# Optimization experiments

Measured on AMD Instinct MI355X. Metric: run time of the kernel, lower is better.

## Reference

```python
import jax, jax.numpy as jnp
import numpy as np

N, DIM, OUT, E = 10000, 256, 256, 320000


def setup_inputs() -> dict:
    key = jax.random.key(0)
    ks = jax.random.split(key, 10)
    def w(k, shape):
        fan_in = shape[0]
        return jax.random.normal(k, shape, jnp.float32) * (fan_in ** -0.5)
    return {
        "v_c": jax.random.normal(ks[0], (N, DIM), jnp.float32),
        # row-normalized-ish random adjacency weights so A @ v stays O(1)
        "A": jax.random.uniform(ks[1], (N, N), jnp.float32) * (2.0 / N),
        "src": jax.random.randint(ks[2], (E,), 0, N, jnp.int32),
        "dst": jax.random.randint(ks[3], (E,), 0, N, jnp.int32),
        # ResidualBlock params: lin1 (dim -> 2dim), lin2 (2dim -> dim)
        "W1": w(ks[4], (DIM, 2 * DIM)), "b1": jnp.zeros((2 * DIM,), jnp.float32),
        "W2": w(ks[5], (2 * DIM, DIM)), "b2": jnp.zeros((DIM,), jnp.float32),
        # LatticeMP_Block lin1 / lin2 (dim -> out_dim)
        "Wl1": w(ks[6], (DIM, OUT)), "bl1": jnp.zeros((OUT,), jnp.float32),
        "Wl2": w(ks[7], (DIM, OUT)), "bl2": jnp.zeros((OUT,), jnp.float32),
    }


def reference(v_c, A, src, dst, W1, b1, W2, b2, Wl1, bl1, Wl2, bl2):
    # ResidualBlock: relu(h + lin2(relu(lin1(h))))
    h1 = jnp.maximum(v_c @ W1 + b1, 0.0) @ W2 + b2          # [N, DIM]
    v = jnp.maximum(v_c + h1, 0.0)                           # [N, DIM]
    # relu(lin1(v)) + relu(lin2(A @ v))
    v = jnp.maximum(v @ Wl1 + bl1, 0.0) + jnp.maximum((A @ v) @ Wl2 + bl2, 0.0)  # [N, OUT]
    # DGL update_all(copy_u, sum): h_N[d] = sum_{(s,d) in E} v[s]
    h_N = jax.ops.segment_sum(v[src], dst, num_segments=N)   # [N, OUT]
    return h_N + v
```

## Files before the change

### kernel.cpp

```cpp
#include <hip/hip_runtime.h>
#include <stdint.h>

#define NN 10000
#define DIMV 256
#define HID 512
#define NEDGE 320000
#define SPLIT 6
#define KCH 1664
#define NKT 313
#define APL 2112
#define ABUF 8448
#define BOFF 16896
#define LDSZ 49664

typedef __attribute__((ext_vector_type(8))) short bf16x8;
typedef __attribute__((ext_vector_type(4))) float f32x4;
typedef __attribute__((ext_vector_type(4))) unsigned short u16x4;
typedef __attribute__((ext_vector_type(2))) unsigned int u32x2;

__device__ __forceinline__ unsigned short f2bf(float f) {
  union { float f; unsigned int u; } c; c.f = f;
  return (unsigned short)((c.u + 0x7FFFu + ((c.u >> 16) & 1u)) >> 16);
}
__device__ __forceinline__ float bf2f(unsigned short h) {
  union { unsigned int u; float f; } c; c.u = ((unsigned int)h) << 16;
  return c.f;
}

__device__ __forceinline__ bf16x8 bzero8() {
  bf16x8 r;
#pragma unroll
  for (int i = 0; i < 8; ++i) r[i] = 0;
  return r;
}

__device__ __forceinline__ bf16x8 pack8(const float* x) {
  bf16x8 r;
#pragma unroll
  for (int i = 0; i < 8; ++i) r[i] = (short)f2bf(x[i]);
  return r;
}

__device__ __forceinline__ u32x2 cvt4v(const f32x4 a) {
  u32x2 r;
  asm("v_cvt_pk_bf16_f32 %0, %1, %2" : "=v"(r[0]) : "v"(a[0]), "v"(a[1]));
  asm("v_cvt_pk_bf16_f32 %0, %1, %2" : "=v"(r[1]) : "v"(a[2]), "v"(a[3]));
  return r;
}

typedef __attribute__((address_space(1))) unsigned int gu32;
typedef __attribute__((address_space(3))) unsigned int lu32;
__device__ __forceinline__ void glds16(const void* g, void* l) {
  __builtin_amdgcn_global_load_lds((const gu32*)g, (lu32*)l, 16, 0, 0);
}

__global__ void k_conv(const float* __restrict__ W1, const float* __restrict__ W2,
                       const float* __restrict__ Wl1, const float* __restrict__ Wl2,
                       unsigned short* __restrict__ W1T, unsigned short* __restrict__ W2T,
                       unsigned short* __restrict__ Wl1T, unsigned short* __restrict__ Wl2T,
                       unsigned short* __restrict__ vB, int* __restrict__ counts) {
  int i = blockIdx.x * 256 + threadIdx.x;
  if (i < 131072) {
    { int k = i >> 9, o = i & 511; W1T[o * 256 + k] = f2bf(W1[i]); }
    { int k = i >> 8, o = i & 255; W2T[o * 512 + k] = f2bf(W2[i]); }
    if (i < 65536) {
      int k = i >> 8, o = i & 255;
      Wl1T[o * 256 + k] = f2bf(Wl1[i]);
      Wl2T[o * 256 + k] = f2bf(Wl2[i]);
    }
    if (i < 4096) {
      int c = i >> 4, kk = 16 + (i & 15);
      int g = kk >> 3;
      int byte = c * 64 + ((g ^ ((c >> 1) & 3)) << 4) + (kk & 7) * 2;
      *(unsigned short*)((char*)vB + (size_t)312 * 16384 + byte) = 0;
    }
    if (i < NN) counts[i] = 0;
  }
}

__launch_bounds__(256, 2)
__global__ void k_mlp(const float* __restrict__ vc,
                      const unsigned short* __restrict__ W1T, const float* __restrict__ b1,
                      const unsigned short* __restrict__ W2T, const float* __restrict__ b2,
                      unsigned short* __restrict__ v_rm, unsigned short* __restrict__ vB) {
  __shared__ __align__(16) char sm[65536];
  const int t = threadIdx.x;
  const int lane = t & 63, wid = t >> 6;
  const int wr = wid & 1, wc = wid >> 1;
  const int r0 = blockIdx.x * 32;

  {
    const int row = t >> 3, grow = r0 + row;
#pragma unroll
    for (int q = 0; q < 4; ++q) {
      const int slot = (t & 7) * 4 + q;
      float buf[8] = {0.f, 0.f, 0.f, 0.f, 0.f, 0.f, 0.f, 0.f};
      if (grow < NN) {
        const float4 x0 = *(const float4*)(vc + (size_t)grow * DIMV + slot * 8);
        const float4 x1 = *(const float4*)(vc + (size_t)grow * DIMV + slot * 8 + 4);
        buf[0] = x0.x; buf[1] = x0.y; buf[2] = x0.z; buf[3] = x0.w;
        buf[4] = x1.x; buf[5] = x1.y; buf[6] = x1.z; buf[7] = x1.w;
      }
      *(bf16x8*)(sm + row * 512 + ((slot ^ (row & 7)) * 16)) = pack8(buf);
    }
  }

  f32x4 acc1[16];
#pragma unroll
  for (int i = 0; i < 16; ++i) acc1[i] = (f32x4){0.f, 0.f, 0.f, 0.f};

  for (int step = 0; step < 8; ++step) {
    __syncthreads();
#pragma unroll
    for (int rr = 0; rr < 2; ++rr) {
      const int c = t + rr * 256;
      const unsigned short* srcp = W1T + c * 256 + step * 32;
#pragma unroll
      for (int q = 0; q < 4; ++q) {
        bf16x8 w = *(const bf16x8*)(srcp + q * 8);
        *(bf16x8*)(sm + 16384 + c * 64 + ((q ^ ((c >> 1) & 3)) * 16)) = w;
      }
    }
    __syncthreads();
    const int arow = 16 * wr + (lane & 15);
    const int aslot = step * 4 + (lane >> 4);
    const bf16x8 af = *(const bf16x8*)(sm + arow * 512 + ((aslot ^ (arow & 7)) * 16));
#pragma unroll
    for (int ct = 0; ct < 16; ++ct) {
      const int c = 256 * wc + 16 * ct + (lane & 15);
      const bf16x8 bfr =
          *(const bf16x8*)(sm + 16384 + c * 64 + ((((lane >> 4)) ^ ((c >> 1) & 3)) * 16));
      acc1[ct] = __builtin_amdgcn_mfma_f32_16x16x32_bf16(af, bfr, acc1[ct], 0, 0, 0);
    }
  }
  __syncthreads();
#pragma unroll
  for (int ct = 0; ct < 16; ++ct) {
    const int c = 256 * wc + 16 * ct + (lane & 15);
    const float bb = b1[c];
#pragma unroll
    for (int r = 0; r < 4; ++r) {
      const int row = 16 * wr + (lane >> 4) * 4 + r;
      float v = fmaxf(acc1[ct][r] + bb, 0.f);
      const int slot = c >> 3;
      *(unsigned short*)(sm + 16384 + row * 1024 + ((slot ^ (row & 7)) * 16) + (c & 7) * 2) =
          f2bf(v);
    }
  }

  f32x4 acc2[8];
#pragma unroll
  for (int i = 0; i < 8; ++i) acc2[i] = (f32x4){0.f, 0.f, 0.f, 0.f};

  for (int step = 0; step < 16; ++step) {
    __syncthreads();
    {
      const int c = t;
      const unsigned short* srcp = W2T + c * 512 + step * 32;
#pragma unroll
      for (int q = 0; q < 4; ++q) {
        bf16x8 w = *(const bf16x8*)(srcp + q * 8);
        *(bf16x8*)(sm + 49152 + c * 64 + ((q ^ ((c >> 1) & 3)) * 16)) = w;
      }
    }
    __syncthreads();
    const int arow = 16 * wr + (lane & 15);
    const int aslot = step * 4 + (lane >> 4);
    const bf16x8 af = *(const bf16x8*)(sm + 16384 + arow * 1024 + ((aslot ^ (arow & 7)) * 16));
#pragma unroll
    for (int ct = 0; ct < 8; ++ct) {
      const int c = 128 * wc + 16 * ct + (lane & 15);
      const bf16x8 bfr =
          *(const bf16x8*)(sm + 49152 + c * 64 + ((((lane >> 4)) ^ ((c >> 1) & 3)) * 16));
      acc2[ct] = __builtin_amdgcn_mfma_f32_16x16x32_bf16(af, bfr, acc2[ct], 0, 0, 0);
    }
  }

  const int growbase = r0 + 16 * wr + (lane >> 4) * 4;
  if (growbase < NN) {
#pragma unroll
    for (int ct = 0; ct < 8; ++ct) {
      const int c = 128 * wc + 16 * ct + (lane & 15);
      const float bb = b2[c];
      u16x4 pk;
#pragma unroll
      for (int r = 0; r < 4; ++r) {
        const int grow = growbase + r;
        float v = acc2[ct][r] + bb + vc[(size_t)grow * DIMV + c];
        v = fmaxf(v, 0.f);
        const unsigned short hv = f2bf(v);
        v_rm[(size_t)grow * DIMV + c] = hv;
        pk[r] = hv;
      }
      const int tile = growbase >> 5, kk0 = growbase & 31;
      const int g = kk0 >> 3;
      const int byte = c * 64 + ((g ^ ((c >> 1) & 3)) << 4) + (kk0 & 7) * 2;
      *(u16x4*)((char*)vB + (size_t)tile * 16384 + byte) = pk;
    }
  }
}

__launch_bounds__(512, 4)
__global__ void k_av(const float* __restrict__ A, const unsigned short* __restrict__ vB,
                     unsigned short* __restrict__ avpb) {
  __shared__ __align__(16) char sm[LDSZ];
  const int t = threadIdx.x, lane = t & 63, wid = t >> 6;
  const int wr = wid >> 2, wc = wid & 3;

  const int orig = blockIdx.x;
  const int xcd = orig & 7, idx = orig >> 3;
  const int g = (xcd < 2) ? xcd * 60 + idx : 120 + (xcd - 2) * 59 + idx;
  const int s = g / 79;
  const int xb = g - s * 79;
  const int r0 = xb * 128;
  const int kbase = s * KCH;
  const int tile0 = s * 52;
  const int nst = (s == SPLIT - 1) ? 53 : 52;
  unsigned short* outp = avpb + (size_t)s * NN * DIMV;

  const int srow = t >> 3, sQ = t & 7;
  const float* ap0 = A + (size_t)min(r0 + srow, NN - 1) * NN;
  const float* ap1 = A + (size_t)min(r0 + 64 + srow, NN - 1) * NN;
  const int wbase = (sQ >> 1) * APL + (sQ & 1) * 8;
  const int w0 = wbase + srow * 16;
  const int w1 = wbase + (64 + srow) * 16;

  f32x4 aR0, aR1;

#define AISSUE(ST)                                            \
  do {                                                        \
    int kq = kbase + (ST)*32 + sQ * 4;                        \
    kq = min(kq, 9996);         \
    aR0 = *(const f32x4*)(ap0 + kq);                          \
    aR1 = *(const f32x4*)(ap1 + kq);                          \
  } while (0)

#define AWRITE(BUF)                                           \
  do {                                                        \
    char* wb = sm + (BUF)*ABUF;                               \
    *(u32x2*)(wb + w0) = cvt4v(aR0);                          \
    *(u32x2*)(wb + w1) = cvt4v(aR1);                          \
  } while (0)

#define BSTAGE(BUF, TILE)                                                     \
  do {                                                                        \
    char* lb = sm + BOFF + (BUF)*16384 + wid * 1024;                          \
    const char* gp = (const char*)vB + (size_t)(TILE)*16384 + wid * 1024 +    \
                     lane * 16;                                               \
    glds16(gp, lb);                                                           \
    glds16(gp + 8192, lb + 8192);                                             \
  } while (0)

  f32x4 acc[4][4];
#pragma unroll
  for (int i = 0; i < 4; ++i)
#pragma unroll
    for (int j = 0; j < 4; ++j) acc[i][j] = (f32x4){0.f, 0.f, 0.f, 0.f};

  const int rbase = (lane >> 4) * APL + (wr * 64 + (lane & 15)) * 16;
  int boff[4];
#pragma unroll
  for (int ct = 0; ct < 4; ++ct) {
    const int col = wc * 64 + ct * 16 + (lane & 15);
    boff[ct] = col * 64 + (((lane >> 4) ^ ((col >> 1) & 3)) << 4);
  }

#define COMPUTE(CUR)                                                                 \
  do {                                                                              \
    const char* ab = sm + (CUR)*ABUF;                                               \
    const char* bb = sm + BOFF + (CUR)*16384;                                       \
    const bf16x8 af0 = *(const bf16x8*)(ab + rbase);                                \
    const bf16x8 af1 = *(const bf16x8*)(ab + rbase + 256);                          \
    const bf16x8 af2 = *(const bf16x8*)(ab + rbase + 512);                          \
    const bf16x8 af3 = *(const bf16x8*)(ab + rbase + 768);                          \
    _Pragma("unroll") for (int ct = 0; ct < 4; ++ct) {                              \
      const bf16x8 bfr = *(const bf16x8*)(bb + boff[ct]);                           \
      acc[0][ct] = __builtin_amdgcn_mfma_f32_16x16x32_bf16(af0, bfr, acc[0][ct], 0, 0, 0); \
      acc[1][ct] = __builtin_amdgcn_mfma_f32_16x16x32_bf16(af1, bfr, acc[1][ct], 0, 0, 0); \
      acc[2][ct] = __builtin_amdgcn_mfma_f32_16x16x32_bf16(af2, bfr, acc[2][ct], 0, 0, 0); \
      acc[3][ct] = __builtin_amdgcn_mfma_f32_16x16x32_bf16(af3, bfr, acc[3][ct], 0, 0, 0); \
    }                                                                               \
  } while (0)

  AISSUE(0);
  AWRITE(0);
  BSTAGE(0, tile0);
  __syncthreads();

  int cur = 0;
  for (int st = 0; st < nst; ++st) {
    const bool more = (st + 1 < nst);
    if (more) {
      AISSUE(st + 1);
      BSTAGE(cur ^ 1, tile0 + st + 1);
    }
    COMPUTE(cur);
    if (more) AWRITE(cur ^ 1);
    __syncthreads();
    cur ^= 1;
  }
#undef AISSUE
#undef AWRITE
#undef BSTAGE
#undef COMPUTE

#pragma unroll
  for (int rt = 0; rt < 4; ++rt) {
    const int gb = r0 + wr * 64 + rt * 16 + (lane >> 4) * 4;
    if (gb < NN) {
#pragma unroll
      for (int ct = 0; ct < 4; ++ct) {
        const int col = wc * 64 + ct * 16 + (lane & 15);
#pragma unroll
        for (int r = 0; r < 4; ++r)
          outp[(size_t)(gb + r) * DIMV + col] = f2bf(acc[rt][ct][r]);
      }
    }
  }
}

__launch_bounds__(256, 2)
__global__ void k_out(const unsigned short* __restrict__ v_rm,
                      const unsigned short* __restrict__ avpb,
                      const unsigned short* __restrict__ Wl1T, const float* __restrict__ bl1,
                      const unsigned short* __restrict__ Wl2T, const float* __restrict__ bl2,
                      unsigned short* __restrict__ v2b, float* __restrict__ outb) {
  __shared__ __align__(16) char sm[65536];
  const int t = threadIdx.x, lane = t & 63, wid = t >> 6;
  const int wr = wid & 1, wc = wid >> 1;
  const int r0 = blockIdx.x * 32;

  {
    const int row = t >> 3, grow = r0 + row;
#pragma unroll
    for (int q = 0; q < 4; ++q) {
      const int slot = (t & 7) * 4 + q;
      bf16x8 w = (grow < NN) ? *(const bf16x8*)(v_rm + (size_t)grow * DIMV + slot * 8) : bzero8();
      *(bf16x8*)(sm + row * 512 + ((slot ^ (row & 7)) * 16)) = w;
    }
#pragma unroll
    for (int q = 0; q < 4; ++q) {
      const int slot = (t & 7) * 4 + q;
      float buf[8] = {0.f, 0.f, 0.f, 0.f, 0.f, 0.f, 0.f, 0.f};
      if (grow < NN) {
#pragma unroll
        for (int p = 0; p < SPLIT; ++p) {
          const bf16x8 a =
              *(const bf16x8*)(avpb + (size_t)p * NN * DIMV + (size_t)grow * DIMV + slot * 8);
#pragma unroll
          for (int z = 0; z < 8; ++z) buf[z] += bf2f((unsigned short)a[z]);
        }
      }
      *(bf16x8*)(sm + 16384 + row * 512 + ((slot ^ (row & 7)) * 16)) = pack8(buf);
    }
  }

  f32x4 acc1[8], acc2[8];
#pragma unroll
  for (int i = 0; i < 8; ++i) {
    acc1[i] = (f32x4){0.f, 0.f, 0.f, 0.f};
    acc2[i] = (f32x4){0.f, 0.f, 0.f, 0.f};
  }

  for (int step = 0; step < 8; ++step) {
    __syncthreads();
    {
      const int c = t;
      const unsigned short* s1 = Wl1T + c * 256 + step * 32;
      const unsigned short* s2 = Wl2T + c * 256 + step * 32;
#pragma unroll
      for (int q = 0; q < 4; ++q) {
        const int ps = (q ^ ((c >> 1) & 3)) * 16;
        *(bf16x8*)(sm + 32768 + c * 64 + ps) = *(const bf16x8*)(s1 + q * 8);
        *(bf16x8*)(sm + 49152 + c * 64 + ps) = *(const bf16x8*)(s2 + q * 8);
      }
    }
    __syncthreads();
    const int arow = 16 * wr + (lane & 15);
    const int aslot = step * 4 + (lane >> 4);
    const bf16x8 a1 = *(const bf16x8*)(sm + arow * 512 + ((aslot ^ (arow & 7)) * 16));
    const bf16x8 a2 = *(const bf16x8*)(sm + 16384 + arow * 512 + ((aslot ^ (arow & 7)) * 16));
#pragma unroll
    for (int ct = 0; ct < 8; ++ct) {
      const int c = 128 * wc + 16 * ct + (lane & 15);
      const int bs = (((lane >> 4)) ^ ((c >> 1) & 3)) * 16;
      acc1[ct] = __builtin_amdgcn_mfma_f32_16x16x32_bf16(
          a1, *(const bf16x8*)(sm + 32768 + c * 64 + bs), acc1[ct], 0, 0, 0);
      acc2[ct] = __builtin_amdgcn_mfma_f32_16x16x32_bf16(
          a2, *(const bf16x8*)(sm + 49152 + c * 64 + bs), acc2[ct], 0, 0, 0);
    }
  }

  const int growbase = r0 + 16 * wr + (lane >> 4) * 4;
  if (growbase < NN) {
#pragma unroll
    for (int ct = 0; ct < 8; ++ct) {
      const int c = 128 * wc + 16 * ct + (lane & 15);
      const float u1 = bl1[c], u2 = bl2[c];
#pragma unroll
      for (int r = 0; r < 4; ++r) {
        const float x = fmaxf(acc1[ct][r] + u1, 0.f) + fmaxf(acc2[ct][r] + u2, 0.f);
        v2b[(size_t)(growbase + r) * DIMV + c] = f2bf(x);
        outb[(size_t)(growbase + r) * DIMV + c] = x;
      }
    }
  }
}

__global__ void k_hist(const int* __restrict__ dst, int* __restrict__ counts) {
  const int e = blockIdx.x * 256 + threadIdx.x;
  if (e < NEDGE) atomicAdd(&counts[dst[e]], 1);
}

__global__ void k_scan(const int* __restrict__ counts, int* __restrict__ offsets,
                       int* __restrict__ cursor) {
  __shared__ int wred[16];
  __shared__ int chtot;
  const int t = threadIdx.x;
  const int lane = t & 63, wid = t >> 6;
  int carry = 0;
  for (int base = 0; base < NN; base += 1024) {
    const int i = base + t;
    const int x = (i < NN) ? counts[i] : 0;
    int v = x;
#pragma unroll
    for (int d = 1; d < 64; d <<= 1) {
      int y = __shfl_up(v, d);
      if (lane >= d) v += y;
    }
    if (lane == 63) wred[wid] = v;
    __syncthreads();
    if (t < 16) {
      int sv = wred[t];
#pragma unroll
      for (int d = 1; d < 16; d <<= 1) {
        int y = __shfl_up(sv, d);
        if (t >= d) sv += y;
      }
      wred[t] = sv;
      if (t == 15) chtot = sv;
    }
    __syncthreads();
    const int woff = wid ? wred[wid - 1] : 0;
    const int excl = carry + woff + v - x;
    if (i < NN) { offsets[i] = excl; cursor[i] = excl; }
    carry += chtot;
    __syncthreads();
  }
  if (t == 0) offsets[NN] = carry;
}

__global__ void k_fill(const int* __restrict__ src, const int* __restrict__ dst,
                       int* __restrict__ cursor, int* __restrict__ srcbuf) {
  const int e = blockIdx.x * 256 + threadIdx.x;
  if (e < NEDGE) {
    const int pos = atomicAdd(&cursor[dst[e]], 1);
    srcbuf[pos] = src[e];
  }
}

__launch_bounds__(256)
__global__ void k_gather(const unsigned short* __restrict__ v2b,
                         const int* __restrict__ offsets,
                         const int* __restrict__ srcbuf, float* __restrict__ outb) {
  const int n = (blockIdx.x * 256 + threadIdx.x) >> 6;
  if (n >= NN) return;
  const int lane = threadIdx.x & 63;
  const int beg = offsets[n], end = offsets[n + 1];
  float4 a0 = {0.f, 0.f, 0.f, 0.f}, a1 = a0, a2 = a0, a3 = a0;
  int j = beg;
  for (; j + 4 <= end; j += 4) {
    const int s0 = srcbuf[j], s1 = srcbuf[j + 1], s2 = srcbuf[j + 2], s3 = srcbuf[j + 3];
    const u16x4 x0 = *(const u16x4*)(v2b + (size_t)s0 * DIMV + lane * 4);
    const u16x4 x1 = *(const u16x4*)(v2b + (size_t)s1 * DIMV + lane * 4);
    const u16x4 x2 = *(const u16x4*)(v2b + (size_t)s2 * DIMV + lane * 4);
    const u16x4 x3 = *(const u16x4*)(v2b + (size_t)s3 * DIMV + lane * 4);
    a0.x += bf2f(x0[0]); a0.y += bf2f(x0[1]); a0.z += bf2f(x0[2]); a0.w += bf2f(x0[3]);
    a1.x += bf2f(x1[0]); a1.y += bf2f(x1[1]); a1.z += bf2f(x1[2]); a1.w += bf2f(x1[3]);
    a2.x += bf2f(x2[0]); a2.y += bf2f(x2[1]); a2.z += bf2f(x2[2]); a2.w += bf2f(x2[3]);
    a3.x += bf2f(x3[0]); a3.y += bf2f(x3[1]); a3.z += bf2f(x3[2]); a3.w += bf2f(x3[3]);
  }
  for (; j < end; ++j) {
    const int s0 = srcbuf[j];
    const u16x4 x0 = *(const u16x4*)(v2b + (size_t)s0 * DIMV + lane * 4);
    a0.x += bf2f(x0[0]); a0.y += bf2f(x0[1]); a0.z += bf2f(x0[2]); a0.w += bf2f(x0[3]);
  }
  a0.x += a1.x + a2.x + a3.x; a0.y += a1.y + a2.y + a3.y;
  a0.z += a1.z + a2.z + a3.z; a0.w += a1.w + a2.w + a3.w;
  float* o = outb + (size_t)n * DIMV + lane * 4;
  float4 cur = *(const float4*)o;
  cur.x += a0.x; cur.y += a0.y; cur.z += a0.z; cur.w += a0.w;
  *(float4*)o = cur;
}

extern "C" void kernel_launch(void* const* d_in, const int* in_sizes, int n_in,
                              void* d_out, int out_size, void* d_ws, size_t ws_size,
                              hipStream_t stream) {
  const float* vc  = (const float*)d_in[0];
  const float* A   = (const float*)d_in[1];
  const int*   src = (const int*)d_in[2];
  const int*   dst = (const int*)d_in[3];
  const float* W1  = (const float*)d_in[4];
  const float* b1  = (const float*)d_in[5];
  const float* W2  = (const float*)d_in[6];
  const float* b2  = (const float*)d_in[7];
  const float* Wl1 = (const float*)d_in[8];
  const float* bl1 = (const float*)d_in[9];
  const float* Wl2 = (const float*)d_in[10];
  const float* bl2 = (const float*)d_in[11];
  float* outb = (float*)d_out;
  char* ws = (char*)d_ws;

  unsigned short* W1T  = (unsigned short*)(ws + 0);
  unsigned short* W2T  = (unsigned short*)(ws + 262144);
  unsigned short* Wl1T = (unsigned short*)(ws + 524288);
  unsigned short* Wl2T = (unsigned short*)(ws + 655360);
  unsigned short* vB   = (unsigned short*)(ws + 786432);
  unsigned short* v_rm = (unsigned short*)(ws + 5914624);
  int* counts  = (int*)(ws + 11034624);
  int* offsets = (int*)(ws + 11075584);
  int* cursor  = (int*)(ws + 11116544);
  int* srcbuf  = (int*)(ws + 11157504);
  unsigned short* avpb = (unsigned short*)(ws + 12437760);
  unsigned short* v2b  = (unsigned short*)(ws + 43157760);

  hipLaunchKernelGGL(k_conv, dim3(512), dim3(256), 0, stream,
                     W1, W2, Wl1, Wl2, W1T, W2T, Wl1T, Wl2T, vB, counts);
  hipLaunchKernelGGL(k_hist, dim3((NEDGE + 255) / 256), dim3(256), 0, stream, dst, counts);
  hipLaunchKernelGGL(k_scan, dim3(1), dim3(1024), 0, stream, counts, offsets, cursor);
  hipLaunchKernelGGL(k_fill, dim3((NEDGE + 255) / 256), dim3(256), 0, stream,
                     src, dst, cursor, srcbuf);
  hipLaunchKernelGGL(k_mlp, dim3(313), dim3(256), 0, stream,
                     vc, W1T, b1, W2T, b2, v_rm, vB);
  hipLaunchKernelGGL(k_av, dim3(474), dim3(512), 0, stream, A, vB, avpb);
  hipLaunchKernelGGL(k_out, dim3(313), dim3(256), 0, stream,
                     v_rm, avpb, Wl1T, bl1, Wl2T, bl2, v2b, outb);
  hipLaunchKernelGGL(k_gather, dim3((NN * 64 + 255) / 256), dim3(256), 0, stream,
                     v2b, offsets, srcbuf, outb);
}
```

Measured before the change: 258.4 us.

## Fold CSR build into MLP, AV and output kernels as extra blocks

```diff
diff --git a/kernel.cpp b/kernel.cpp
--- a/kernel.cpp
+++ b/kernel.cpp
@@ -82,7 +82,13 @@
 __global__ void k_mlp(const float* __restrict__ vc,
                       const unsigned short* __restrict__ W1T, const float* __restrict__ b1,
                       const unsigned short* __restrict__ W2T, const float* __restrict__ b2,
-                      unsigned short* __restrict__ v_rm, unsigned short* __restrict__ vB) {
+                      unsigned short* __restrict__ v_rm, unsigned short* __restrict__ vB,
+                      const int* __restrict__ dst, int* __restrict__ counts) {
+  if (blockIdx.x >= 313) {
+    const int e0 = (blockIdx.x - 313) * 256 + threadIdx.x;
+    for (int e = e0; e < NEDGE; e += 40 * 256) atomicAdd(&counts[dst[e]], 1);
+    return;
+  }
   __shared__ __align__(16) char sm[65536];
   const int t = threadIdx.x;
   const int lane = t & 63, wid = t >> 6;
@@ -202,9 +208,45 @@
 
 __launch_bounds__(512, 4)
 __global__ void k_av(const float* __restrict__ A, const unsigned short* __restrict__ vB,
-                     unsigned short* __restrict__ avpb) {
+                     unsigned short* __restrict__ avpb,
+                     const int* __restrict__ counts, int* __restrict__ offsets,
+                     int* __restrict__ cursor) {
   __shared__ __align__(16) char sm[LDSZ];
   const int t = threadIdx.x, lane = t & 63, wid = t >> 6;
+
+  if (blockIdx.x >= 474) {
+    int* wred = (int*)sm;
+    int carry = 0;
+    for (int base = 0; base < NN; base += 512) {
+      const int i = base + t;
+      const int x = (i < NN) ? counts[i] : 0;
+      int v = x;
+#pragma unroll
+      for (int d = 1; d < 64; d <<= 1) {
+        int y = __shfl_up(v, d);
+        if (lane >= d) v += y;
+      }
+      if (lane == 63) wred[wid] = v;
+      __syncthreads();
+      if (t < 8) {
+        int sv = wred[t];
+#pragma unroll
+        for (int d = 1; d < 8; d <<= 1) {
+          int y = __shfl_up(sv, d);
+          if (t >= d) sv += y;
+        }
+        wred[t] = sv;
+      }
+      __syncthreads();
+      const int excl = carry + (wid ? wred[wid - 1] : 0) + v - x;
+      if (i < NN) { offsets[i] = excl; cursor[i] = excl; }
+      carry += wred[7];
+      __syncthreads();
+    }
+    if (t == 0) offsets[NN] = carry;
+    return;
+  }
+
   const int wr = wid >> 2, wc = wid & 3;
 
   const int orig = blockIdx.x;
@@ -324,7 +366,17 @@
                       const unsigned short* __restrict__ avpb,
                       const unsigned short* __restrict__ Wl1T, const float* __restrict__ bl1,
                       const unsigned short* __restrict__ Wl2T, const float* __restrict__ bl2,
-                      unsigned short* __restrict__ v2b, float* __restrict__ outb) {
+                      unsigned short* __restrict__ v2b, float* __restrict__ outb,
+                      const int* __restrict__ src, const int* __restrict__ dst,
+                      int* __restrict__ cursor, int* __restrict__ srcbuf) {
+  if (blockIdx.x >= 313) {
+    const int e0 = (blockIdx.x - 313) * 256 + threadIdx.x;
+    for (int e = e0; e < NEDGE; e += 40 * 256) {
+      const int pos = atomicAdd(&cursor[dst[e]], 1);
+      srcbuf[pos] = src[e];
+    }
+    return;
+  }
   __shared__ __align__(16) char sm[65536];
   const int t = threadIdx.x, lane = t & 63, wid = t >> 6;
   const int wr = wid & 1, wc = wid >> 1;
@@ -404,58 +456,6 @@
         outb[(size_t)(growbase + r) * DIMV + c] = x;
       }
     }
-  }
-}
-
-__global__ void k_hist(const int* __restrict__ dst, int* __restrict__ counts) {
-  const int e = blockIdx.x * 256 + threadIdx.x;
-  if (e < NEDGE) atomicAdd(&counts[dst[e]], 1);
-}
-
-__global__ void k_scan(const int* __restrict__ counts, int* __restrict__ offsets,
-                       int* __restrict__ cursor) {
-  __shared__ int wred[16];
-  __shared__ int chtot;
-  const int t = threadIdx.x;
-  const int lane = t & 63, wid = t >> 6;
-  int carry = 0;
-  for (int base = 0; base < NN; base += 1024) {
-    const int i = base + t;
-    const int x = (i < NN) ? counts[i] : 0;
-    int v = x;
-#pragma unroll
-    for (int d = 1; d < 64; d <<= 1) {
-      int y = __shfl_up(v, d);
-      if (lane >= d) v += y;
-    }
-    if (lane == 63) wred[wid] = v;
-    __syncthreads();
-    if (t < 16) {
-      int sv = wred[t];
-#pragma unroll
-      for (int d = 1; d < 16; d <<= 1) {
-        int y = __shfl_up(sv, d);
-        if (t >= d) sv += y;
-      }
-      wred[t] = sv;
-      if (t == 15) chtot = sv;
-    }
-    __syncthreads();
-    const int woff = wid ? wred[wid - 1] : 0;
-    const int excl = carry + woff + v - x;
-    if (i < NN) { offsets[i] = excl; cursor[i] = excl; }
-    carry += chtot;
-    __syncthreads();
-  }
-  if (t == 0) offsets[NN] = carry;
-}
-
-__global__ void k_fill(const int* __restrict__ src, const int* __restrict__ dst,
-                       int* __restrict__ cursor, int* __restrict__ srcbuf) {
-  const int e = blockIdx.x * 256 + threadIdx.x;
-  if (e < NEDGE) {
-    const int pos = atomicAdd(&cursor[dst[e]], 1);
-    srcbuf[pos] = src[e];
   }
 }
 
@@ -468,25 +468,37 @@
   const int lane = threadIdx.x & 63;
   const int beg = offsets[n], end = offsets[n + 1];
   float4 a0 = {0.f, 0.f, 0.f, 0.f}, a1 = a0, a2 = a0, a3 = a0;
+  float4 a4 = a0, a5 = a0, a6 = a0, a7 = a0;
   int j = beg;
-  for (; j + 4 <= end; j += 4) {
+  for (; j + 8 <= end; j += 8) {
     const int s0 = srcbuf[j], s1 = srcbuf[j + 1], s2 = srcbuf[j + 2], s3 = srcbuf[j + 3];
+    const int s4 = srcbuf[j + 4], s5 = srcbuf[j + 5], s6 = srcbuf[j + 6], s7 = srcbuf[j + 7];
     const u16x4 x0 = *(const u16x4*)(v2b + (size_t)s0 * DIMV + lane * 4);
     const u16x4 x1 = *(const u16x4*)(v2b + (size_t)s1 * DIMV + lane * 4);
     const u16x4 x2 = *(const u16x4*)(v2b + (size_t)s2 * DIMV + lane * 4);
     const u16x4 x3 = *(const u16x4*)(v2b + (size_t)s3 * DIMV + lane * 4);
+    const u16x4 x4 = *(const u16x4*)(v2b + (size_t)s4 * DIMV + lane * 4);
+    const u16x4 x5 = *(const u16x4*)(v2b + (size_t)s5 * DIMV + lane * 4);
+    const u16x4 x6 = *(const u16x4*)(v2b + (size_t)s6 * DIMV + lane * 4);
+    const u16x4 x7 = *(const u16x4*)(v2b + (size_t)s7 * DIMV + lane * 4);
     a0.x += bf2f(x0[0]); a0.y += bf2f(x0[1]); a0.z += bf2f(x0[2]); a0.w += bf2f(x0[3]);
     a1.x += bf2f(x1[0]); a1.y += bf2f(x1[1]); a1.z += bf2f(x1[2]); a1.w += bf2f(x1[3]);
     a2.x += bf2f(x2[0]); a2.y += bf2f(x2[1]); a2.z += bf2f(x2[2]); a2.w += bf2f(x2[3]);
     a3.x += bf2f(x3[0]); a3.y += bf2f(x3[1]); a3.z += bf2f(x3[2]); a3.w += bf2f(x3[3]);
+    a4.x += bf2f(x4[0]); a4.y += bf2f(x4[1]); a4.z += bf2f(x4[2]); a4.w += bf2f(x4[3]);
+    a5.x += bf2f(x5[0]); a5.y += bf2f(x5[1]); a5.z += bf2f(x5[2]); a5.w += bf2f(x5[3]);
+    a6.x += bf2f(x6[0]); a6.y += bf2f(x6[1]); a6.z += bf2f(x6[2]); a6.w += bf2f(x6[3]);
+    a7.x += bf2f(x7[0]); a7.y += bf2f(x7[1]); a7.z += bf2f(x7[2]); a7.w += bf2f(x7[3]);
   }
   for (; j < end; ++j) {
     const int s0 = srcbuf[j];
     const u16x4 x0 = *(const u16x4*)(v2b + (size_t)s0 * DIMV + lane * 4);
     a0.x += bf2f(x0[0]); a0.y += bf2f(x0[1]); a0.z += bf2f(x0[2]); a0.w += bf2f(x0[3]);
   }
-  a0.x += a1.x + a2.x + a3.x; a0.y += a1.y + a2.y + a3.y;
-  a0.z += a1.z + a2.z + a3.z; a0.w += a1.w + a2.w + a3.w;
+  a0.x += a1.x + a2.x + a3.x + a4.x + a5.x + a6.x + a7.x;
+  a0.y += a1.y + a2.y + a3.y + a4.y + a5.y + a6.y + a7.y;
+  a0.z += a1.z + a2.z + a3.z + a4.z + a5.z + a6.z + a7.z;
+  a0.w += a1.w + a2.w + a3.w + a4.w + a5.w + a6.w + a7.w;
   float* o = outb + (size_t)n * DIMV + lane * 4;
   float4 cur = *(const float4*)o;
   cur.x += a0.x; cur.y += a0.y; cur.z += a0.z; cur.w += a0.w;
@@ -526,15 +538,13 @@
 
   hipLaunchKernelGGL(k_conv, dim3(512), dim3(256), 0, stream,
                      W1, W2, Wl1, Wl2, W1T, W2T, Wl1T, Wl2T, vB, counts);
-  hipLaunchKernelGGL(k_hist, dim3((NEDGE + 255) / 256), dim3(256), 0, stream, dst, counts);
-  hipLaunchKernelGGL(k_scan, dim3(1), dim3(1024), 0, stream, counts, offsets, cursor);
-  hipLaunchKernelGGL(k_fill, dim3((NEDGE + 255) / 256), dim3(256), 0, stream,
+  hipLaunchKernelGGL(k_mlp, dim3(353), dim3(256), 0, stream,
+                     vc, W1T, b1, W2T, b2, v_rm, vB, dst, counts);
+  hipLaunchKernelGGL(k_av, dim3(475), dim3(512), 0, stream,
+                     A, vB, avpb, counts, offsets, cursor);
+  hipLaunchKernelGGL(k_out, dim3(353), dim3(256), 0, stream,
+                     v_rm, avpb, Wl1T, bl1, Wl2T, bl2, v2b, outb,
                      src, dst, cursor, srcbuf);
-  hipLaunchKernelGGL(k_mlp, dim3(313), dim3(256), 0, stream,
-                     vc, W1T, b1, W2T, b2, v_rm, vB);
-  hipLaunchKernelGGL(k_av, dim3(474), dim3(512), 0, stream, A, vB, avpb);
-  hipLaunchKernelGGL(k_out, dim3(313), dim3(256), 0, stream,
-                     v_rm, avpb, Wl1T, bl1, Wl2T, bl2, v2b, outb);
   hipLaunchKernelGGL(k_gather, dim3((NN * 64 + 255) / 256), dim3(256), 0, stream,
                      v2b, offsets, srcbuf, outb);
 }
```

New measurement: 236.6 us. 8.4% less time.
